# Optimization experiments

Hardware: AMD Instinct MI355X
Metric: run time of the kernel (lower is better)

## Reference

```python
import jax, jax.numpy as jnp
import numpy as np

N = 100000
D_FEAT = 256
HID = 128
EMB = 64
FANOUT = 16


def setup_inputs() -> dict:
    key = jax.random.key(0)
    k = jax.random.split(key, 7)
    s = 0.05
    features = jax.random.normal(k[0], (N, D_FEAT), dtype=jnp.float32)
    W1 = jax.random.normal(k[1], (HID, 2 * D_FEAT), dtype=jnp.float32) * s
    W2 = jax.random.normal(k[2], (HID, 2 * HID), dtype=jnp.float32) * s
    W3 = jax.random.normal(k[3], (HID, 2 * HID), dtype=jnp.float32) * s
    W4 = jax.random.normal(k[4], (EMB, 2 * HID), dtype=jnp.float32) * s
    nodes = jnp.arange(N, dtype=jnp.int32)
    neigh = jax.random.randint(k[5], (N, FANOUT), 0, N, dtype=jnp.int32)
    return {"features": features, "W1": W1, "W2": W2, "W3": W3, "W4": W4,
            "nodes": nodes, "neigh": neigh}


def _sage_layer(h, neigh, W):
    # MeanAggregator: mean of sampled neighbor features  [N, d]
    neigh_mean = jnp.mean(h[neigh], axis=1)
    # Encoder (gcn=False): relu(W @ cat([self, neigh_mean]).T) -> [N, out]
    combined = jnp.concatenate([h, neigh_mean], axis=1)  # [N, 2d]
    return jax.nn.relu(combined @ W.T)


def reference(features, W1, W2, W3, W4, nodes, neigh):
    h1 = _sage_layer(features, neigh, W1)  # [N, HID]
    h2 = _sage_layer(h1, neigh, W2)        # [N, HID]
    h3 = _sage_layer(h2, neigh, W3)        # [N, HID]
    h4 = _sage_layer(h3, neigh, W4)        # [N, EMB]
    # GraphEmbeddingModule.forward returns gSAGE4(n).t() -> [len(n), EMB]
    return h4[nodes]
```

## Files before the change

kernel.cpp:

```cpp
#include <hip/hip_runtime.h>
#include <hip/hip_bf16.h>


constexpr int N_NODES = 100000;
constexpr int FANOUT  = 16;

typedef __attribute__((ext_vector_type(8))) short short8;
typedef __attribute__((ext_vector_type(4))) float f32x4;

__device__ inline unsigned short bf16_rne(float f) {
    unsigned u = __float_as_uint(f);
    return (unsigned short)((u + 0x7fffu + ((u >> 16) & 1u)) >> 16);
}
__device__ inline float bf16_tof(unsigned short s) {
    return __uint_as_float(((unsigned)s) << 16);
}

__global__ __launch_bounds__(256)
void prep_Bsw(const float* __restrict__ W, unsigned short* __restrict__ Bhi,
              unsigned short* __restrict__ Blo, int D_IN, int D_OUT)
{
    int i = blockIdx.x * 256 + threadIdx.x;
    int total = 2 * D_OUT * D_IN;
    if (i >= total) return;
    int K = D_IN, C = 2 * D_OUT;
    int c = i / K, k = i % K;
    float v = (c < D_OUT) ? W[(size_t)c * (2 * K) + k]
                          : W[(size_t)(c - D_OUT) * (2 * K) + K + k];
    int tc = c >> 4, mlc = c & 15;
    int tk = k >> 5, qk = (k >> 3) & 3, e = k & 7;
    size_t off = ((size_t)(tk * (C / 16) + tc) * 64 + qk * 16 + mlc) * 8 + e;
    unsigned short hi = bf16_rne(v);
    Bhi[off] = hi;
    Blo[off] = bf16_rne(v - bf16_tof(hi));
}

__global__ __launch_bounds__(256, 3)
void gemm1(const float* __restrict__ hf,
           const unsigned short* __restrict__ Bhi,
           const unsigned short* __restrict__ Blo,
           float* __restrict__ gs, unsigned short* __restrict__ gn, int N)
{
    constexpr int K = 256, DO = 128, LDA = 40;
    __shared__ unsigned short Ah[64 * LDA], Al[64 * LDA];

    const int tid  = threadIdx.x;
    const int wave = tid >> 6;
    const int lane = tid & 63;
    const int ml   = lane & 15;
    const int quad = lane >> 4;
    const int node0 = blockIdx.x * 64;

    const int srow = tid >> 3;
    const int sc4  = tid & 7;
    int nd0 = node0 + srow;      if (nd0 >= N) nd0 = N - 1;
    int nd1 = node0 + srow + 32; if (nd1 >= N) nd1 = N - 1;
    const float* pA0 = &hf[(size_t)nd0 * K + sc4 * 4];
    const float* pA1 = &hf[(size_t)nd1 * K + sc4 * 4];

    f32x4 acc[4][4];
    #pragma unroll
    for (int mi = 0; mi < 4; ++mi)
        #pragma unroll
        for (int ni = 0; ni < 4; ++ni)
            acc[mi][ni] = (f32x4){0.f, 0.f, 0.f, 0.f};

    float4 pf0 = *(const float4*)&pA0[0];
    float4 pf1 = *(const float4*)&pA1[0];

    for (int k0 = 0; k0 < K; k0 += 32) {
        {
            float v0[4] = {pf0.x, pf0.y, pf0.z, pf0.w};
            float v1[4] = {pf1.x, pf1.y, pf1.z, pf1.w};
            unsigned short h0[4], l0[4], h1[4], l1[4];
            #pragma unroll
            for (int e = 0; e < 4; ++e) {
                h0[e] = bf16_rne(v0[e]); l0[e] = bf16_rne(v0[e] - bf16_tof(h0[e]));
                h1[e] = bf16_rne(v1[e]); l1[e] = bf16_rne(v1[e] - bf16_tof(h1[e]));
            }
            *(uint2*)&Ah[srow * LDA + sc4 * 4]        = *(const uint2*)h0;
            *(uint2*)&Al[srow * LDA + sc4 * 4]        = *(const uint2*)l0;
            *(uint2*)&Ah[(srow + 32) * LDA + sc4 * 4] = *(const uint2*)h1;
            *(uint2*)&Al[(srow + 32) * LDA + sc4 * 4] = *(const uint2*)l1;
        }
        if (k0 + 32 < K) {
            pf0 = *(const float4*)&pA0[k0 + 32];
            pf1 = *(const float4*)&pA1[k0 + 32];
        }
        __syncthreads();

        short8 afh[4], afl[4];
        #pragma unroll
        for (int mi = 0; mi < 4; ++mi) {
            int r = mi * 16 + ml;
            afh[mi] = *(const short8*)&Ah[r * LDA + quad * 8];
            afl[mi] = *(const short8*)&Al[r * LDA + quad * 8];
        }
        const size_t bbase = (size_t)((k0 >> 5) * 16 + wave * 4) * 512 + (size_t)lane * 8;
        #pragma unroll
        for (int ni = 0; ni < 4; ++ni) {
            short8 bh = *(const short8*)&Bhi[bbase + ni * 512];
            short8 bl = *(const short8*)&Blo[bbase + ni * 512];
            #pragma unroll
            for (int mi = 0; mi < 4; ++mi) {
                acc[mi][ni] = __builtin_amdgcn_mfma_f32_16x16x32_bf16(afl[mi], bh, acc[mi][ni], 0, 0, 0);
                acc[mi][ni] = __builtin_amdgcn_mfma_f32_16x16x32_bf16(afh[mi], bl, acc[mi][ni], 0, 0, 0);
                acc[mi][ni] = __builtin_amdgcn_mfma_f32_16x16x32_bf16(afh[mi], bh, acc[mi][ni], 0, 0, 0);
            }
        }
        __syncthreads();
    }

    #pragma unroll
    for (int mi = 0; mi < 4; ++mi)
        #pragma unroll
        for (int r = 0; r < 4; ++r) {
            int node = node0 + mi * 16 + quad * 4 + r;
            if (node >= N) continue;
            #pragma unroll
            for (int ni = 0; ni < 4; ++ni) {
                int c = wave * 64 + ni * 16 + ml;
                float v = acc[mi][ni][r];
                if (c < DO) gs[(size_t)node * DO + c] = v;
                else        gn[(size_t)node * DO + (c - DO)] = bf16_rne(v);
            }
        }
}

template<int C>
__global__ __launch_bounds__(256, 4)
void fused_layer(const float* __restrict__ gs_in,
                 const unsigned short* __restrict__ gn_in,
                 const int* __restrict__ neigh,
                 const unsigned short* __restrict__ Bhi,
                 const unsigned short* __restrict__ Blo,
                 float* __restrict__ gs_out,
                 unsigned short* __restrict__ gn_out, int N)
{
    constexpr int K = 128, DO = C / 2, NI = C / 64, LDAF = 136;
    __shared__ unsigned short Afh[64 * LDAF], Afl[64 * LDAF];

    const int tid  = threadIdx.x;
    const int wave = tid >> 6;
    const int lane = tid & 63;
    const int ml   = lane & 15;
    const int quad = lane >> 4;
    const int node0 = blockIdx.x * 64;

    {
        const int row = tid >> 2;
        const int seg = tid & 3;
        int nd = node0 + row; if (nd >= N) nd = N - 1;
        const int4* nb4 = (const int4*)(neigh + (size_t)nd * FANOUT);
        int4 q0 = nb4[0], q1 = nb4[1], q2 = nb4[2], q3 = nb4[3];
        int ids[FANOUT] = {q0.x, q0.y, q0.z, q0.w, q1.x, q1.y, q1.z, q1.w,
                           q2.x, q2.y, q2.z, q2.w, q3.x, q3.y, q3.z, q3.w};
        float acc[32];
        #pragma unroll
        for (int c = 0; c < 32; ++c) acc[c] = 0.f;
        #pragma unroll
        for (int j = 0; j < FANOUT; ++j) {
            const uint4* src = (const uint4*)&gn_in[(size_t)ids[j] * 128 + seg * 32];
            #pragma unroll
            for (int t = 0; t < 4; ++t) {
                uint4 q = src[t];
                acc[t*8+0] += __uint_as_float(q.x << 16);
                acc[t*8+1] += __uint_as_float(q.x & 0xffff0000u);
                acc[t*8+2] += __uint_as_float(q.y << 16);
                acc[t*8+3] += __uint_as_float(q.y & 0xffff0000u);
                acc[t*8+4] += __uint_as_float(q.z << 16);
                acc[t*8+5] += __uint_as_float(q.z & 0xffff0000u);
                acc[t*8+6] += __uint_as_float(q.w << 16);
                acc[t*8+7] += __uint_as_float(q.w & 0xffff0000u);
            }
        }
        const float inv = 1.0f / (float)FANOUT;
        alignas(16) unsigned short th[32], tl[32];
        const float4* gsp = (const float4*)&gs_in[(size_t)nd * 128 + seg * 32];
        #pragma unroll
        for (int t = 0; t < 8; ++t) {
            float4 s = gsp[t];
            float sv[4] = {s.x, s.y, s.z, s.w};
            #pragma unroll
            for (int e = 0; e < 4; ++e) {
                float h = fmaxf(fmaf(acc[t*4+e], inv, sv[e]), 0.f);
                unsigned short hi = bf16_rne(h);
                th[t*4+e] = hi;
                tl[t*4+e] = bf16_rne(h - bf16_tof(hi));
            }
        }
        #pragma unroll
        for (int t = 0; t < 4; ++t) {
            *(uint4*)&Afh[row * LDAF + seg * 32 + t * 8] = *(const uint4*)&th[t * 8];
            *(uint4*)&Afl[row * LDAF + seg * 32 + t * 8] = *(const uint4*)&tl[t * 8];
        }
    }
    __syncthreads();

    f32x4 acc[4][NI];
    #pragma unroll
    for (int mi = 0; mi < 4; ++mi)
        #pragma unroll
        for (int ni = 0; ni < NI; ++ni)
            acc[mi][ni] = (f32x4){0.f, 0.f, 0.f, 0.f};

    for (int k0 = 0; k0 < K; k0 += 32) {
        short8 afh[4], afl[4];
        #pragma unroll
        for (int mi = 0; mi < 4; ++mi) {
            int r = mi * 16 + ml;
            afh[mi] = *(const short8*)&Afh[r * LDAF + k0 + quad * 8];
            afl[mi] = *(const short8*)&Afl[r * LDAF + k0 + quad * 8];
        }
        const size_t bbase = (size_t)((k0 >> 5) * (C / 16) + wave * NI) * 512 + (size_t)lane * 8;
        #pragma unroll
        for (int ni = 0; ni < NI; ++ni) {
            short8 bh = *(const short8*)&Bhi[bbase + ni * 512];
            short8 bl = *(const short8*)&Blo[bbase + ni * 512];
            #pragma unroll
            for (int mi = 0; mi < 4; ++mi) {
                acc[mi][ni] = __builtin_amdgcn_mfma_f32_16x16x32_bf16(afl[mi], bh, acc[mi][ni], 0, 0, 0);
                acc[mi][ni] = __builtin_amdgcn_mfma_f32_16x16x32_bf16(afh[mi], bl, acc[mi][ni], 0, 0, 0);
                acc[mi][ni] = __builtin_amdgcn_mfma_f32_16x16x32_bf16(afh[mi], bh, acc[mi][ni], 0, 0, 0);
            }
        }
    }

    #pragma unroll
    for (int mi = 0; mi < 4; ++mi)
        #pragma unroll
        for (int r = 0; r < 4; ++r) {
            int node = node0 + mi * 16 + quad * 4 + r;
            if (node >= N) continue;
            #pragma unroll
            for (int ni = 0; ni < NI; ++ni) {
                int c = wave * (16 * NI) + ni * 16 + ml;
                float v = acc[mi][ni][r];
                if (c < DO) gs_out[(size_t)node * DO + c] = v;
                else        gn_out[(size_t)node * DO + (c - DO)] = bf16_rne(v);
            }
        }
}

__global__ __launch_bounds__(256)
void agg_out(const float* __restrict__ gs4, const unsigned short* __restrict__ gn4,
             const int* __restrict__ neigh, const int* __restrict__ nodes,
             float* __restrict__ out, int N)
{
    const int i    = blockIdx.x * 32 + (threadIdx.x >> 3);
    const int lane = threadIdx.x & 7;
    if (i >= N) return;
    const int nd = nodes[i];
    const int4* nb4 = (const int4*)(neigh + (size_t)nd * FANOUT);
    int4 q0 = nb4[0], q1 = nb4[1], q2 = nb4[2], q3 = nb4[3];
    int ids[FANOUT] = {q0.x, q0.y, q0.z, q0.w, q1.x, q1.y, q1.z, q1.w,
                       q2.x, q2.y, q2.z, q2.w, q3.x, q3.y, q3.z, q3.w};
    float acc[8];
    #pragma unroll
    for (int c = 0; c < 8; ++c) acc[c] = 0.f;
    #pragma unroll
    for (int j = 0; j < FANOUT; ++j) {
        uint4 q = *(const uint4*)&gn4[(size_t)ids[j] * 64 + lane * 8];
        acc[0] += __uint_as_float(q.x << 16);
        acc[1] += __uint_as_float(q.x & 0xffff0000u);
        acc[2] += __uint_as_float(q.y << 16);
        acc[3] += __uint_as_float(q.y & 0xffff0000u);
        acc[4] += __uint_as_float(q.z << 16);
        acc[5] += __uint_as_float(q.z & 0xffff0000u);
        acc[6] += __uint_as_float(q.w << 16);
        acc[7] += __uint_as_float(q.w & 0xffff0000u);
    }
    const float inv = 1.0f / (float)FANOUT;
    const float* s = gs4 + (size_t)nd * 64 + lane * 8;
    float4 s0 = *(const float4*)&s[0];
    float4 s1 = *(const float4*)&s[4];
    float4 o0, o1;
    o0.x = fmaxf(fmaf(acc[0], inv, s0.x), 0.f);
    o0.y = fmaxf(fmaf(acc[1], inv, s0.y), 0.f);
    o0.z = fmaxf(fmaf(acc[2], inv, s0.z), 0.f);
    o0.w = fmaxf(fmaf(acc[3], inv, s0.w), 0.f);
    o1.x = fmaxf(fmaf(acc[4], inv, s1.x), 0.f);
    o1.y = fmaxf(fmaf(acc[5], inv, s1.y), 0.f);
    o1.z = fmaxf(fmaf(acc[6], inv, s1.z), 0.f);
    o1.w = fmaxf(fmaf(acc[7], inv, s1.w), 0.f);
    float* op = out + (size_t)i * 64 + lane * 8;
    *(float4*)&op[0] = o0;
    *(float4*)&op[4] = o1;
}

extern "C" void kernel_launch(void* const* d_in, const int* in_sizes, int n_in,
                              void* d_out, int out_size, void* d_ws, size_t ws_size,
                              hipStream_t stream)
{
    const float* features = (const float*)d_in[0];
    const float* W1       = (const float*)d_in[1];
    const float* W2       = (const float*)d_in[2];
    const float* W3       = (const float*)d_in[3];
    const float* W4       = (const float*)d_in[4];
    const int*   nodes    = (const int*)d_in[5];
    const int*   neigh    = (const int*)d_in[6];
    float*       out      = (float*)d_out;

    unsigned short* B1h = (unsigned short*)d_ws;
    unsigned short* B1l = B1h + 65536;
    unsigned short* B2h = B1l + 65536;
    unsigned short* B2l = B2h + 32768;
    unsigned short* B3h = B2l + 32768;
    unsigned short* B3l = B3h + 32768;
    unsigned short* B4h = B3l + 32768;
    unsigned short* B4l = B4h + 16384;
    float* gs = (float*)(B4l + 16384);
    unsigned short* gnA = (unsigned short*)(gs + (size_t)N_NODES * 128);
    unsigned short* gnB = gnA + (size_t)N_NODES * 128;
    float* gs4 = (float*)gnB;
    unsigned short* gn4 = gnB + (size_t)N_NODES * 128;

    prep_Bsw<<<(65536 + 255) / 256, 256, 0, stream>>>(W1, B1h, B1l, 256, 128);
    prep_Bsw<<<(32768 + 255) / 256, 256, 0, stream>>>(W2, B2h, B2l, 128, 128);
    prep_Bsw<<<(32768 + 255) / 256, 256, 0, stream>>>(W3, B3h, B3l, 128, 128);
    prep_Bsw<<<(16384 + 255) / 256, 256, 0, stream>>>(W4, B4h, B4l, 128, 64);

    const int grid = (N_NODES + 63) / 64;

    gemm1<<<grid, 256, 0, stream>>>(features, B1h, B1l, gs, gnA, N_NODES);
    fused_layer<256><<<grid, 256, 0, stream>>>(gs, gnA, neigh, B2h, B2l, gs, gnB, N_NODES);
    fused_layer<256><<<grid, 256, 0, stream>>>(gs, gnB, neigh, B3h, B3l, gs, gnA, N_NODES);
    fused_layer<128><<<grid, 256, 0, stream>>>(gs, gnA, neigh, B4h, B4l, gs4, gn4, N_NODES);
    agg_out<<<(N_NODES + 31) / 32, 256, 0, stream>>>(gs4, gn4, neigh, nodes, out, N_NODES);
}
```

Before: 488.2 us.

## Interleave gather segments, XOR-swizzle LDS tile, raise occupancy hint

The neighbor gather now has the four threads of a row read adjacent 16-byte chunks, so each load instruction touches contiguous 64-byte spans instead of strided pieces. The padded LDS A tile is replaced by an unpadded one with an XOR swizzle on the column offset, which shrinks shared memory and still avoids bank conflicts on the MFMA fragment reads. Launch bounds go from 4 to 5 blocks per CU, which may force register spilling in exchange for more waves to hide gather latency.

```diff
diff --git a/kernel.cpp b/kernel.cpp
--- a/kernel.cpp
+++ b/kernel.cpp
@@ -128,7 +128,7 @@
 }
 
 template<int C>
-__global__ __launch_bounds__(256, 4)
+__global__ __launch_bounds__(256, 5)
 void fused_layer(const float* __restrict__ gs_in,
                  const unsigned short* __restrict__ gn_in,
                  const int* __restrict__ neigh,
@@ -137,8 +137,8 @@
                  float* __restrict__ gs_out,
                  unsigned short* __restrict__ gn_out, int N)
 {
-    constexpr int K = 128, DO = C / 2, NI = C / 64, LDAF = 136;
-    __shared__ unsigned short Afh[64 * LDAF], Afl[64 * LDAF];
+    constexpr int K = 128, DO = C / 2, NI = C / 64;
+    __shared__ unsigned short Afh[64 * 128], Afl[64 * 128];
 
     const int tid  = threadIdx.x;
     const int wave = tid >> 6;
@@ -160,10 +160,10 @@
         for (int c = 0; c < 32; ++c) acc[c] = 0.f;
         #pragma unroll
         for (int j = 0; j < FANOUT; ++j) {
-            const uint4* src = (const uint4*)&gn_in[(size_t)ids[j] * 128 + seg * 32];
+            const uint4* src = (const uint4*)&gn_in[(size_t)ids[j] * 128];
             #pragma unroll
             for (int t = 0; t < 4; ++t) {
-                uint4 q = src[t];
+                uint4 q = src[4 * t + seg];
                 acc[t*8+0] += __uint_as_float(q.x << 16);
                 acc[t*8+1] += __uint_as_float(q.x & 0xffff0000u);
                 acc[t*8+2] += __uint_as_float(q.y << 16);
@@ -175,24 +175,23 @@
             }
         }
         const float inv = 1.0f / (float)FANOUT;
-        alignas(16) unsigned short th[32], tl[32];
-        const float4* gsp = (const float4*)&gs_in[(size_t)nd * 128 + seg * 32];
-        #pragma unroll
-        for (int t = 0; t < 8; ++t) {
-            float4 s = gsp[t];
-            float sv[4] = {s.x, s.y, s.z, s.w};
-            #pragma unroll
-            for (int e = 0; e < 4; ++e) {
-                float h = fmaxf(fmaf(acc[t*4+e], inv, sv[e]), 0.f);
+        const float* gsp = &gs_in[(size_t)nd * 128];
+        #pragma unroll
+        for (int t = 0; t < 4; ++t) {
+            float4 s0 = *(const float4*)&gsp[32 * t + 8 * seg];
+            float4 s1 = *(const float4*)&gsp[32 * t + 8 * seg + 4];
+            float sv[8] = {s0.x, s0.y, s0.z, s0.w, s1.x, s1.y, s1.z, s1.w};
+            alignas(16) unsigned short th[8], tl[8];
+            #pragma unroll
+            for (int e = 0; e < 8; ++e) {
+                float h = fmaxf(fmaf(acc[t*8+e], inv, sv[e]), 0.f);
                 unsigned short hi = bf16_rne(h);
-                th[t*4+e] = hi;
-                tl[t*4+e] = bf16_rne(h - bf16_tof(hi));
-            }
-        }
-        #pragma unroll
-        for (int t = 0; t < 4; ++t) {
-            *(uint4*)&Afh[row * LDAF + seg * 32 + t * 8] = *(const uint4*)&th[t * 8];
-            *(uint4*)&Afl[row * LDAF + seg * 32 + t * 8] = *(const uint4*)&tl[t * 8];
+                th[e] = hi;
+                tl[e] = bf16_rne(h - bf16_tof(hi));
+            }
+            int soff = (row * 128 + 32 * t + 8 * seg) ^ ((row & 7) << 3);
+            *(uint4*)&Afh[soff] = *(const uint4*)th;
+            *(uint4*)&Afl[soff] = *(const uint4*)tl;
         }
     }
     __syncthreads();
@@ -209,8 +208,9 @@
         #pragma unroll
         for (int mi = 0; mi < 4; ++mi) {
             int r = mi * 16 + ml;
-            afh[mi] = *(const short8*)&Afh[r * LDAF + k0 + quad * 8];
-            afl[mi] = *(const short8*)&Afl[r * LDAF + k0 + quad * 8];
+            int soff = (r * 128 + k0 + quad * 8) ^ ((r & 7) << 3);
+            afh[mi] = *(const short8*)&Afh[soff];
+            afl[mi] = *(const short8*)&Afl[soff];
         }
         const size_t bbase = (size_t)((k0 >> 5) * (C / 16) + wave * NI) * 512 + (size_t)lane * 8;
         #pragma unroll
```

After: 551.6 us. 13.0% more time.
